# Performance work log

Measured on AMD Instinct MI355X. Metric: run time of the kernel, lower is better.

The kernel has to match this reference:

```python
import jax, jax.numpy as jnp
import numpy as np

R = 8
EPS = 1e-08


def diff_x(t, r):
    # t: (B,C,H,W), running cumsum along H -> windowed sum along H
    left = t[:, :, r:2 * r + 1]
    middle = t[:, :, 2 * r + 1:] - t[:, :, :-2 * r - 1]
    right = t[:, :, -1:] - t[:, :, -2 * r - 1:-r - 1]
    return jnp.concatenate([left, middle, right], axis=2)


def diff_y(t, r):
    left = t[:, :, :, r:2 * r + 1]
    middle = t[:, :, :, 2 * r + 1:] - t[:, :, :, :-2 * r - 1]
    right = t[:, :, :, -1:] - t[:, :, :, -2 * r - 1:-r - 1]
    return jnp.concatenate([left, middle, right], axis=3)


def box_filter(x, r):
    return diff_y(diff_x(jnp.cumsum(x, axis=2), r).cumsum(axis=3), r)


def bilinear_align_corners(x, H, W):
    # x: (B,C,h,w) -> (B,C,H,W), matching F.interpolate(mode='bilinear', align_corners=True)
    h, w = x.shape[2], x.shape[3]
    ys = jnp.linspace(0.0, h - 1.0, H, dtype=x.dtype)
    xs = jnp.linspace(0.0, w - 1.0, W, dtype=x.dtype)
    y0 = jnp.clip(jnp.floor(ys).astype(jnp.int32), 0, h - 1)
    x0 = jnp.clip(jnp.floor(xs).astype(jnp.int32), 0, w - 1)
    y1 = jnp.clip(y0 + 1, 0, h - 1)
    x1 = jnp.clip(x0 + 1, 0, w - 1)
    wy = (ys - y0.astype(x.dtype))[:, None]   # (H,1)
    wx = (xs - x0.astype(x.dtype))[None, :]   # (1,W)
    v00 = x[:, :, y0[:, None], x0[None, :]]
    v01 = x[:, :, y0[:, None], x1[None, :]]
    v10 = x[:, :, y1[:, None], x0[None, :]]
    v11 = x[:, :, y1[:, None], x1[None, :]]
    top = v00 * (1 - wx) + v01 * wx
    bot = v10 * (1 - wx) + v11 * wx
    return top * (1 - wy) + bot * wy


def setup_inputs() -> dict:
    key = jax.random.key(0)
    k1, k2, k3 = jax.random.split(key, 3)
    lr_x = jax.random.uniform(k1, (4, 3, 512, 512), dtype=jnp.float32)
    lr_y = jax.random.uniform(k2, (4, 3, 512, 512), dtype=jnp.float32)
    hr_x = jax.random.uniform(k3, (4, 3, 2048, 2048), dtype=jnp.float32)
    return {"lr_x": lr_x, "lr_y": lr_y, "hr_x": hr_x}


def reference(lr_x, lr_y, hr_x):
    _, _, h_lr, w_lr = lr_x.shape
    _, _, h_hr, w_hr = hr_x.shape
    N = box_filter(jnp.ones((1, 1, h_lr, w_lr), dtype=lr_x.dtype), R)
    mean_x = box_filter(lr_x, R) / N
    mean_y = box_filter(lr_y, R) / N
    cov_xy = box_filter(lr_x * lr_y, R) / N - mean_x * mean_y
    var_x = box_filter(lr_x * lr_x, R) / N - mean_x * mean_x
    A = cov_xy / (var_x + EPS)
    b = mean_y - A * mean_x
    mean_A = bilinear_align_corners(A, h_hr, w_hr)
    mean_b = bilinear_align_corners(b, h_hr, w_hr)
    return mean_A * hr_x + mean_b
```

## Files before the change

### kernel.cpp

```cpp
#include <hip/hip_runtime.h>

#define RR 8
#define TILE 32
#define EXT (TILE + 2 * RR)

typedef float f4 __attribute__((ext_vector_type(4)));

__global__ __launch_bounds__(256) void k_ab(
    const float* __restrict__ lrx, const float* __restrict__ lry,
    float2* __restrict__ ABout, int H, int W) {
  __shared__ float sx[EXT][EXT];
  __shared__ float sy[EXT][EXT];
  __shared__ float hx[EXT][TILE];
  __shared__ float hy[EXT][TILE];
  __shared__ float hxy[EXT][TILE];
  __shared__ float hxx[EXT][TILE];

  const int bc = blockIdx.z;
  const size_t plane = (size_t)bc * H * W;
  const float* __restrict__ px = lrx + plane;
  const float* __restrict__ py = lry + plane;
  const int tx0 = blockIdx.x * TILE;
  const int ty0 = blockIdx.y * TILE;
  const int tid = threadIdx.y * 32 + threadIdx.x;

  const bool interior = (tx0 >= RR) && (ty0 >= RR) &&
                        (tx0 + TILE + RR <= W) && (ty0 + TILE + RR <= H);
  if (interior) {
    const size_t base = (size_t)(ty0 - RR) * W + (tx0 - RR);
    for (int i = tid; i < EXT * (EXT / 4); i += 256) {
      int r = i / (EXT / 4);
      int c4 = (i - r * (EXT / 4)) * 4;
      size_t o = base + (size_t)r * W + c4;
      *(float4*)&sx[r][c4] = *(const float4*)(px + o);
      *(float4*)&sy[r][c4] = *(const float4*)(py + o);
    }
  } else {
    for (int i = tid; i < EXT * EXT; i += 256) {
      int r = i / EXT, c = i % EXT;
      int gy = ty0 + r - RR, gx = tx0 + c - RR;
      float vx = 0.f, vy = 0.f;
      if (gy >= 0 && gy < H && gx >= 0 && gx < W) {
        size_t o = (size_t)gy * W + gx;
        vx = px[o];
        vy = py[o];
      }
      sx[r][c] = vx;
      sy[r][c] = vy;
    }
  }
  __syncthreads();

  for (int q = tid; q < EXT * (TILE / 4); q += 256) {
    int r = q >> 3;
    int c0 = (q & 7) * 4;
    float xv[20], yv[20];
#pragma unroll
    for (int t = 0; t < 5; ++t) {
      float4 x4 = *(const float4*)&sx[r][c0 + 4 * t];
      float4 y4 = *(const float4*)&sy[r][c0 + 4 * t];
      xv[4 * t + 0] = x4.x; xv[4 * t + 1] = x4.y; xv[4 * t + 2] = x4.z; xv[4 * t + 3] = x4.w;
      yv[4 * t + 0] = y4.x; yv[4 * t + 1] = y4.y; yv[4 * t + 2] = y4.z; yv[4 * t + 3] = y4.w;
    }
    float pv[20], qv[20];
#pragma unroll
    for (int i = 0; i < 20; ++i) { pv[i] = xv[i] * yv[i]; qv[i] = xv[i] * xv[i]; }
    float ax = 0.f, ay = 0.f, axy = 0.f, axx = 0.f;
#pragma unroll
    for (int i = 0; i < 17; ++i) { ax += xv[i]; ay += yv[i]; axy += pv[i]; axx += qv[i]; }
    float4 ox, oy, oxy, oxx;
    ox.x = ax; oy.x = ay; oxy.x = axy; oxx.x = axx;
#pragma unroll
    for (int j = 1; j < 4; ++j) {
      ax += xv[j + 16] - xv[j - 1];
      ay += yv[j + 16] - yv[j - 1];
      axy += pv[j + 16] - pv[j - 1];
      axx += qv[j + 16] - qv[j - 1];
      (&ox.x)[j] = ax; (&oy.x)[j] = ay; (&oxy.x)[j] = axy; (&oxx.x)[j] = axx;
    }
    *(float4*)&hx[r][c0] = ox;
    *(float4*)&hy[r][c0] = oy;
    *(float4*)&hxy[r][c0] = oxy;
    *(float4*)&hxx[r][c0] = oxx;
  }
  __syncthreads();

  const int c = threadIdx.x;
  const int r0 = threadIdx.y * 4;
  float vx[20], vy[20], vxy[20], vxx[20];
#pragma unroll
  for (int i = 0; i < 20; ++i) {
    vx[i] = hx[r0 + i][c];
    vy[i] = hy[r0 + i][c];
    vxy[i] = hxy[r0 + i][c];
    vxx[i] = hxx[r0 + i][c];
  }
  float sX = 0.f, sY = 0.f, sXY = 0.f, sXX = 0.f;
#pragma unroll
  for (int i = 0; i < 17; ++i) { sX += vx[i]; sY += vy[i]; sXY += vxy[i]; sXX += vxx[i]; }

  const int gx = tx0 + c;
  const int nx = min(gx + RR, W - 1) - max(gx - RR, 0) + 1;
#pragma unroll
  for (int j = 0; j < 4; ++j) {
    if (j > 0) {
      sX += vx[j + 16] - vx[j - 1];
      sY += vy[j + 16] - vy[j - 1];
      sXY += vxy[j + 16] - vxy[j - 1];
      sXX += vxx[j + 16] - vxx[j - 1];
    }
    const int gy = ty0 + r0 + j;
    const int ny = min(gy + RR, H - 1) - max(gy - RR, 0) + 1;
    float inv = 1.f / (float)(nx * ny);
    float mx = sX * inv;
    float my = sY * inv;
    float cov = sXY * inv - mx * my;
    float var = sXX * inv - mx * mx;
    float a = cov / (var + 1e-8f);
    float bv = my - a * mx;
    size_t o = plane + (size_t)gy * W + gx;
    ABout[o] = make_float2(a, bv);
  }
}

#define ROWS 8
#define KO_LDSW 264
__global__ __launch_bounds__(256) void k_out(
    const float2* __restrict__ AB, const float* __restrict__ hr,
    float* __restrict__ out, int hl, int wl, int Hh, int Wh) {
  __shared__ float2 ABs[4][KO_LDSW];

  const int yb = blockIdx.y * ROWS;
  const int bc = blockIdx.z;
  const int xb = blockIdx.x * 1024;

  const float scy = (float)(hl - 1) / (float)(Hh - 1);
  const float scx = (float)(wl - 1) / (float)(Wh - 1);

  int v = (int)((float)yb * scy);
  if (v > hl - 1) v = hl - 1;

  const int x0base = (int)((float)xb * scx);
  const size_t lrBase = (size_t)bc * hl * wl;

  for (int i = threadIdx.x; i < 4 * KO_LDSW; i += 256) {
    int rr = i / KO_LDSW;
    int cc = i - rr * KO_LDSW;
    int xl = x0base + cc;
    if (xl > wl - 1) xl = wl - 1;
    int yr = v + rr;
    if (yr > hl - 1) yr = hl - 1;
    ABs[rr][cc] = AB[lrBase + (size_t)yr * wl + xl];
  }

  const int xg = xb + threadIdx.x * 4;
  int li[4];
  float wxv[4];
#pragma unroll
  for (int j = 0; j < 4; ++j) {
    float fx = (float)(xg + j) * scx;
    int x0 = (int)fx;
    wxv[j] = fx - (float)x0;
    li[j] = x0 - x0base;
  }

  const size_t hrBase = ((size_t)bc * Hh + yb) * Wh + xg;
  f4 h[ROWS];
#pragma unroll
  for (int r = 0; r < ROWS; ++r)
    h[r] = __builtin_nontemporal_load((const f4*)(hr + hrBase + (size_t)r * Wh));

  __syncthreads();

#pragma unroll
  for (int r = 0; r < ROWS; ++r) {
    float fy = (float)(yb + r) * scy;
    int y0 = (int)fy;
    if (y0 > hl - 1) y0 = hl - 1;
    int y1 = y0 + 1;
    if (y1 > hl - 1) y1 = hl - 1;
    const float wy = fy - (float)y0;
    const float2* __restrict__ R0 = ABs[y0 - v];
    const float2* __restrict__ R1 = ABs[y1 - v];
    f4 res;
#pragma unroll
    for (int j = 0; j < 4; ++j) {
      int l = li[j];
      float w = wxv[j];
      float2 p00 = R0[l], p01 = R0[l + 1];
      float2 p10 = R1[l], p11 = R1[l + 1];
      float at = p00.x + (p01.x - p00.x) * w;
      float ab = p10.x + (p11.x - p10.x) * w;
      float bt = p00.y + (p01.y - p00.y) * w;
      float bb = p10.y + (p11.y - p10.y) * w;
      float a = at + (ab - at) * wy;
      float b = bt + (bb - bt) * wy;
      res[j] = a * h[r][j] + b;
    }
    *(f4*)(out + hrBase + (size_t)r * Wh) = res;
  }
}

extern "C" void kernel_launch(void* const* d_in, const int* in_sizes, int n_in,
                              void* d_out, int out_size, void* d_ws, size_t ws_size,
                              hipStream_t stream) {
  const float* lrx = (const float*)d_in[0];
  const float* lry = (const float*)d_in[1];
  const float* hrx = (const float*)d_in[2];
  float* out = (float*)d_out;

  const int BC = 12;
  const int hl = 512, wl = 512;
  const int Hh = 2048, Wh = 2048;

  float2* AB = (float2*)d_ws;

  dim3 g1(wl / TILE, hl / TILE, BC);
  dim3 b1(32, 8);
  k_ab<<<g1, b1, 0, stream>>>(lrx, lry, AB, hl, wl);

  dim3 g2(Wh / 1024, Hh / ROWS, BC);
  dim3 b2(256);
  k_out<<<g2, b2, 0, stream>>>(AB, hrx, out, hl, wl, Hh, Wh);
}
```

Baseline: 364.0 us.

## Halve rows per block, reuse LDS taps across lanes, use nontemporal stores

The output kernel now handles 4 high-res rows per block instead of 8, which doubles the grid and shrinks the LDS staging to 3 low-res rows. Each thread reads 3 float2 taps per low-res row once and selects between them per output pixel, instead of doing 4 separate 2x2 gathers, so LDS traffic drops. Output writes switch to nontemporal stores to avoid polluting the cache. In exchange, blocks re-stage more AB rows overall, and the tap selection assumes each thread's 4 pixels span at most 3 low-res columns.

```diff
diff --git a/kernel.cpp b/kernel.cpp
--- a/kernel.cpp
+++ b/kernel.cpp
@@ -123,16 +123,17 @@
   }
 }
 
-#define ROWS 8
+#define ROWS 4
 #define KO_LDSW 264
 __global__ __launch_bounds__(256) void k_out(
     const float2* __restrict__ AB, const float* __restrict__ hr,
     float* __restrict__ out, int hl, int wl, int Hh, int Wh) {
-  __shared__ float2 ABs[4][KO_LDSW];
+  __shared__ float2 ABs[3][KO_LDSW];
 
   const int yb = blockIdx.y * ROWS;
   const int bc = blockIdx.z;
   const int xb = blockIdx.x * 1024;
+  const int tid = threadIdx.x;
 
   const float scy = (float)(hl - 1) / (float)(Hh - 1);
   const float scx = (float)(wl - 1) / (float)(Wh - 1);
@@ -140,10 +141,24 @@
   int v = (int)((float)yb * scy);
   if (v > hl - 1) v = hl - 1;
 
+  int ry0[ROWS], ry1[ROWS];
+  float wyv[ROWS];
+#pragma unroll
+  for (int r = 0; r < ROWS; ++r) {
+    float fy = (float)(yb + r) * scy;
+    int y0 = (int)fy;
+    if (y0 > hl - 1) y0 = hl - 1;
+    int y1 = y0 + 1;
+    if (y1 > hl - 1) y1 = hl - 1;
+    wyv[r] = fy - (float)y0;
+    ry0[r] = y0 - v;
+    ry1[r] = y1 - v;
+  }
+
   const int x0base = (int)((float)xb * scx);
   const size_t lrBase = (size_t)bc * hl * wl;
 
-  for (int i = threadIdx.x; i < 4 * KO_LDSW; i += 256) {
+  for (int i = tid; i < 3 * KO_LDSW; i += 256) {
     int rr = i / KO_LDSW;
     int cc = i - rr * KO_LDSW;
     int xl = x0base + cc;
@@ -153,15 +168,23 @@
     ABs[rr][cc] = AB[lrBase + (size_t)yr * wl + xl];
   }
 
-  const int xg = xb + threadIdx.x * 4;
-  int li[4];
+  const int xg = xb + tid * 4;
   float wxv[4];
-#pragma unroll
-  for (int j = 0; j < 4; ++j) {
-    float fx = (float)(xg + j) * scx;
-    int x0 = (int)fx;
-    wxv[j] = fx - (float)x0;
-    li[j] = x0 - x0base;
+  int dsel[4];
+  int l0;
+  {
+    float fx0 = (float)xg * scx;
+    int x00 = (int)fx0;
+    l0 = x00 - x0base;
+    wxv[0] = fx0 - (float)x00;
+    dsel[0] = 0;
+#pragma unroll
+    for (int j = 1; j < 4; ++j) {
+      float fx = (float)(xg + j) * scx;
+      int x0 = (int)fx;
+      wxv[j] = fx - (float)x0;
+      dsel[j] = x0 - x00;
+    }
   }
 
   const size_t hrBase = ((size_t)bc * Hh + yb) * Wh + xg;
@@ -174,30 +197,30 @@
 
 #pragma unroll
   for (int r = 0; r < ROWS; ++r) {
-    float fy = (float)(yb + r) * scy;
-    int y0 = (int)fy;
-    if (y0 > hl - 1) y0 = hl - 1;
-    int y1 = y0 + 1;
-    if (y1 > hl - 1) y1 = hl - 1;
-    const float wy = fy - (float)y0;
-    const float2* __restrict__ R0 = ABs[y0 - v];
-    const float2* __restrict__ R1 = ABs[y1 - v];
+    const float2* __restrict__ R0 = ABs[ry0[r]];
+    const float2* __restrict__ R1 = ABs[ry1[r]];
+    const float wy = wyv[r];
+    float2 q00 = R0[l0], q01 = R0[l0 + 1], q02 = R0[l0 + 2];
+    float2 q10 = R1[l0], q11 = R1[l0 + 1], q12 = R1[l0 + 2];
+    float w0a = q00.x + (q10.x - q00.x) * wy;
+    float w0b = q00.y + (q10.y - q00.y) * wy;
+    float w1a = q01.x + (q11.x - q01.x) * wy;
+    float w1b = q01.y + (q11.y - q01.y) * wy;
+    float w2a = q02.x + (q12.x - q02.x) * wy;
+    float w2b = q02.y + (q12.y - q02.y) * wy;
     f4 res;
 #pragma unroll
     for (int j = 0; j < 4; ++j) {
-      int l = li[j];
+      float loa = dsel[j] ? w1a : w0a;
+      float lob = dsel[j] ? w1b : w0b;
+      float hia = dsel[j] ? w2a : w1a;
+      float hib = dsel[j] ? w2b : w1b;
       float w = wxv[j];
-      float2 p00 = R0[l], p01 = R0[l + 1];
-      float2 p10 = R1[l], p11 = R1[l + 1];
-      float at = p00.x + (p01.x - p00.x) * w;
-      float ab = p10.x + (p11.x - p10.x) * w;
-      float bt = p00.y + (p01.y - p00.y) * w;
-      float bb = p10.y + (p11.y - p10.y) * w;
-      float a = at + (ab - at) * wy;
-      float b = bt + (bb - bt) * wy;
+      float a = loa + (hia - loa) * w;
+      float b = lob + (hib - lob) * w;
       res[j] = a * h[r][j] + b;
     }
-    *(f4*)(out + hrBase + (size_t)r * Wh) = res;
+    __builtin_nontemporal_store(res, (f4*)(out + hrBase + (size_t)r * Wh));
   }
 }
 
```

New measurement: 359.0 us. No clear change (-1.4%).
